# Optimization experiments

Measured on AMD Instinct MI355X. Metric: run time of the kernel, lower is better.

The kernel has to match this reference:

```python
import jax, jax.numpy as jnp
import numpy as np

N = 50000       # num_nodes
E = 800000      # num_edges (avg degree 16)
DIN = 128       # input_dim
DOUT = 128      # output_dim
H = 4           # num_heads
HD = DOUT // H  # head_dim = 32


def setup_inputs() -> dict:
    key = jax.random.key(0)
    ks = jax.random.split(key, 9)
    x = jax.random.normal(ks[0], (N, DIN), dtype=jnp.float32)
    edge_index = jax.random.randint(ks[1], (2, E), 0, N, dtype=jnp.int64)
    s = 1.0 / np.sqrt(DIN)
    Wq = jax.random.uniform(ks[2], (DOUT, DIN), jnp.float32, -s, s)
    bq = jax.random.uniform(ks[3], (DOUT,), jnp.float32, -s, s)
    Wk = jax.random.uniform(ks[4], (DOUT, DIN), jnp.float32, -s, s)
    bk = jax.random.uniform(ks[5], (DOUT,), jnp.float32, -s, s)
    Wv = jax.random.uniform(ks[6], (DOUT, DIN), jnp.float32, -s, s)
    bv = jax.random.uniform(ks[7], (DOUT,), jnp.float32, -s, s)
    att = jax.random.normal(ks[8], (H, 2 * HD), dtype=jnp.float32)  # nn.Parameter(randn)
    return {"x": x, "edge_index": edge_index, "Wq": Wq, "bq": bq,
            "Wk": Wk, "bk": bk, "Wv": Wv, "bv": bv, "att": att}


def reference(x, edge_index, Wq, bq, Wk, bk, Wv, bv, att):
    n = x.shape[0]
    q = (x @ Wq.T + bq).reshape(n, H, HD)
    k = (x @ Wk.T + bk).reshape(n, H, HD)
    v = (x @ Wv.T + bv).reshape(n, H, HD)
    row, col = edge_index[0], edge_index[1]

    # scores = leaky_relu(sum(cat([q[row],k[col]]) * att)) computed without concat
    a_q, a_k = att[:, :HD], att[:, HD:]                       # [H,HD] each
    scores = jnp.einsum('ehd,hd->eh', q[row], a_q) \
           + jnp.einsum('ehd,hd->eh', k[col], a_k)            # [E,H]
    scores = jax.nn.leaky_relu(scores, 0.2)

    # segment-softmax over edges grouped by destination node (col), per head
    m = jax.ops.segment_max(scores, col, num_segments=n)      # [N,H]
    m = jnp.where(jnp.isfinite(m), m, 0.0)                    # empty segments -> -inf guard
    e = jnp.exp(scores - m[col])                              # [E,H]
    denom = jax.ops.segment_sum(e, col, num_segments=n)       # [N,H]
    w_edge = e / denom[col]                                   # softmax per dst segment

    # attention_weights[i] = mean over incoming edges of softmax weights; 0 if deg==0
    deg = jax.ops.segment_sum(jnp.ones((col.shape[0],), jnp.float32), col,
                              num_segments=n)                 # [N]
    w_sum = jax.ops.segment_sum(w_edge, col, num_segments=n)  # [N,H]
    attn_w = jnp.where(deg[:, None] > 0, w_sum / jnp.maximum(deg, 1.0)[:, None], 0.0)

    # output[dst] += attn_w[dst] * v[src], summed over edges
    msgs = attn_w[col][:, :, None] * v[row]                   # [E,H,HD]
    out = jax.ops.segment_sum(msgs, col, num_segments=n)      # [N,H,HD]
    return out.reshape(n, DOUT)                               # dropout: eval mode (identity)
```

## Files before the change

### kernel.cpp

```cpp
#include <hip/hip_runtime.h>


#define N_NODES 50000
#define N_EDGES 800000
#define SPAN    96
#define NBUCK   521
#define CAP     2304
#define HSPAN   48
#define EPB     2048
#define NCHUNK  391
#define GEMMB   391

#define OFF_SORTED 12800000
#define OFF_CURSOR 17601536

typedef __attribute__((ext_vector_type(8))) short short8;
typedef __attribute__((ext_vector_type(4))) float f32x4;

__device__ __forceinline__ unsigned int pack_bf16_rne(float a, float b) {
    unsigned int ua = __float_as_uint(a), ub = __float_as_uint(b);
    unsigned int ha = (ua + 0x7FFFu + ((ua >> 16) & 1u)) >> 16;
    unsigned int hb = (ub + 0x7FFFu + ((ub >> 16) & 1u)) >> 16;
    return ha | (hb << 16);
}
__device__ __forceinline__ unsigned short bf16_rne(float a) {
    unsigned int ua = __float_as_uint(a);
    return (unsigned short)((ua + 0x7FFFu + ((ua >> 16) & 1u)) >> 16);
}
__device__ __forceinline__ float bflo(unsigned int u) { return __uint_as_float(u << 16); }
__device__ __forceinline__ float bfhi(unsigned int u) { return __uint_as_float(u & 0xFFFF0000u); }

__global__ __launch_bounds__(512) void fused_gemm_scatter(
        const float* __restrict__ x, const float* __restrict__ Wv,
        const float* __restrict__ bv, unsigned int* __restrict__ vh,
        const int* __restrict__ ei, unsigned int* __restrict__ Cursor,
        unsigned int* __restrict__ sorted) {
    __shared__ __align__(16) unsigned char smem[128 * 68 * 4];
    __shared__ int s_wide;
    int t = threadIdx.x;

    if (blockIdx.x < GEMMB) {
        unsigned int* wB = (unsigned int*)smem;
        for (int q = t; q < 8192; q += 512) {
            int o = q >> 6, k2 = q & 63;
            float2 wp = ((const float2*)Wv)[q];
            wB[o * 68 + k2] = pack_bf16_rne(wp.x, wp.y);
        }
        __syncthreads();

        int lane = t & 63, w = t >> 6;
        int quad = lane >> 4, lc = lane & 15;
        int n0 = blockIdx.x * 128 + w * 16;

        int arow = n0 + lc;
        int arowc = min(arow, N_NODES - 1);
        const float4* xrow = (const float4*)(x + (size_t)arowc * 128);

        f32x4 acc[8];
        #pragma unroll
        for (int ot = 0; ot < 8; ++ot) acc[ot] = (f32x4){0.f, 0.f, 0.f, 0.f};

        #pragma unroll
        for (int ks = 0; ks < 4; ++ks) {
            float4 f0 = xrow[ks * 8 + quad * 2];
            float4 f1 = xrow[ks * 8 + quad * 2 + 1];
            uint4 a4;
            a4.x = pack_bf16_rne(f0.x, f0.y);
            a4.y = pack_bf16_rne(f0.z, f0.w);
            a4.z = pack_bf16_rne(f1.x, f1.y);
            a4.w = pack_bf16_rne(f1.z, f1.w);
            short8 af = *(const short8*)&a4;
            #pragma unroll
            for (int ot = 0; ot < 8; ++ot) {
                uint4 b4 = *(const uint4*)&wB[(ot * 16 + lc) * 68 + ks * 16 + quad * 4];
                short8 bf = *(const short8*)&b4;
                acc[ot] = __builtin_amdgcn_mfma_f32_16x16x32_bf16(af, bf, acc[ot], 0, 0, 0);
            }
        }

        #pragma unroll
        for (int ot = 0; ot < 8; ++ot) {
            int o = ot * 16 + lc;
            float bb = bv[o];
            #pragma unroll
            for (int r = 0; r < 4; ++r) {
                int node = n0 + quad * 4 + r;
                unsigned short u = bf16_rne(acc[ot][r] + bb);
                unsigned int partner = (unsigned int)__shfl_xor((int)u, 1, 64);
                if ((lane & 1) == 0 && node < N_NODES) {
                    unsigned int pair = (unsigned int)u | (partner << 16);
                    vh[(size_t)node * 64 + (o >> 1)] = pair;
                }
            }
        }
    } else {
        unsigned int* w = (unsigned int*)smem;
        int* h    = (int*)(smem + EPB * 4);
        int* base = (int*)(smem + EPB * 4 + NBUCK * 4);
        unsigned int V = Cursor[NBUCK];
        for (int j = t; j < NBUCK; j += 512) h[j] = 0;
        if (t < 64) {
            int nz = (ei[2 * t + 1] != 0) ? 1 : 0;
            unsigned long long b = __ballot(nz);
            if (t == 0) s_wide = (b == 0ULL) ? 1 : 0;
        }
        __syncthreads();
        int wide = s_wide;
        int e0 = (blockIdx.x - GEMMB) * EPB;

        #pragma unroll
        for (int k = 0; k < EPB / 512; ++k) {
            int e = e0 + k * 512 + t;
            if (e < N_EDGES) {
                int r, c;
                if (wide) {
                    r = (int)((const uint2*)ei)[e].x;
                    c = (int)((const uint2*)ei)[N_EDGES + e].x;
                } else {
                    r = ei[e];
                    c = ei[N_EDGES + e];
                }
                w[k * 512 + t] = ((unsigned int)c << 16) | (unsigned int)r;
                atomicAdd(&h[c / SPAN], 1);
            } else {
                w[k * 512 + t] = 0xFFFFFFFFu;
            }
        }
        __syncthreads();
        for (int j = t; j < NBUCK; j += 512) {
            int cnt = h[j];
            base[j] = cnt ? (int)(atomicAdd(&Cursor[j], (unsigned int)cnt) - V) : 0;
            h[j] = 0;
        }
        __syncthreads();
        #pragma unroll
        for (int k = 0; k < EPB / 512; ++k) {
            unsigned int ww = w[k * 512 + t];
            if (ww != 0xFFFFFFFFu) {
                int bin = (int)(ww >> 16) / SPAN;
                int p = base[bin] + atomicAdd(&h[bin], 1);
                if (p >= 0 && p < CAP)
                    sorted[(size_t)bin * CAP + p] = ww;
            }
        }
    }
}

__global__ __launch_bounds__(512) void gather_kernel(const unsigned int* __restrict__ vh,
                                                     const unsigned int* __restrict__ sorted,
                                                     const unsigned int* __restrict__ Cursor,
                                                     float* __restrict__ out,
                                                     int ch) {
    __shared__ unsigned int ww[CAP];
    __shared__ unsigned short rl[CAP];
    __shared__ int deg[HSPAN];
    __shared__ int startc[HSPAN];
    __shared__ int curp[HSPAN];
    int t = threadIdx.x;
    int b  = blockIdx.x >> 1;
    int hb = blockIdx.x & 1;
    int nb0 = b * SPAN + hb * HSPAN;
    int span = min(HSPAN, N_NODES - nb0);
    if (span <= 0) return;
    unsigned int V = Cursor[NBUCK];
    int cnt = min((int)(Cursor[b] - V), CAP);
    if (t < HSPAN) deg[t] = 0;
    __syncthreads();

    const unsigned int* run = sorted + (size_t)b * CAP;
    for (int i = t; i < cnt; i += 512) {
        unsigned int v = run[i];
        ww[i] = v;
        unsigned int ln = (v >> 16) - (unsigned int)nb0;
        if (ln < (unsigned int)HSPAN) atomicAdd(&deg[ln], 1);
    }
    __syncthreads();

    if (t < 64) {
        int v = (t < HSPAN) ? deg[t] : 0;
        int s = v;
        #pragma unroll
        for (int off = 1; off < 64; off <<= 1) {
            int y = __shfl_up(s, off, 64);
            if (t >= off) s += y;
        }
        if (t < HSPAN) { startc[t] = s - v; curp[t] = 0; }
    }
    __syncthreads();

    for (int i = t; i < cnt; i += 512) {
        unsigned int v = ww[i];
        unsigned int ln = (v >> 16) - (unsigned int)nb0;
        if (ln < (unsigned int)HSPAN) {
            int p = startc[ln] + atomicAdd(&curp[ln], 1);
            rl[p] = (unsigned short)(v & 0xFFFFu);
        }
    }
    __syncthreads();

    int lane = t & 63, wid = t >> 6;
    int quad = lane >> 4;
    int li = lane & 15;
    const uint2* v2 = (const uint2*)(vh + (size_t)ch * 32);

#define ACC4(p) do { \
        c0 += (double)bflo((p).x); c1 += (double)bfhi((p).x); \
        c2 += (double)bflo((p).y); c3 += (double)bfhi((p).y); } while (0)

    for (int g = wid; g * 4 < span; g += 8) {
        int ln = g * 4 + quad;
        int s0 = startc[ln], d = deg[ln];
        double c0 = 0., c1 = 0., c2 = 0., c3 = 0.;
        int j = 0;
        if (d >= 8) {
            int a0 = rl[s0 + 0], a1 = rl[s0 + 1];
            int a2 = rl[s0 + 2], a3 = rl[s0 + 3];
            uint2 pA0 = v2[(size_t)a0 * 32 + li];
            uint2 pA1 = v2[(size_t)a1 * 32 + li];
            uint2 pA2 = v2[(size_t)a2 * 32 + li];
            uint2 pA3 = v2[(size_t)a3 * 32 + li];
            for (; j + 8 <= d; j += 4) {
                int b0 = rl[s0 + j + 4], b1 = rl[s0 + j + 5];
                int b2 = rl[s0 + j + 6], b3 = rl[s0 + j + 7];
                uint2 pB0 = v2[(size_t)b0 * 32 + li];
                uint2 pB1 = v2[(size_t)b1 * 32 + li];
                uint2 pB2 = v2[(size_t)b2 * 32 + li];
                uint2 pB3 = v2[(size_t)b3 * 32 + li];
                ACC4(pA0); ACC4(pA1); ACC4(pA2); ACC4(pA3);
                pA0 = pB0; pA1 = pB1; pA2 = pB2; pA3 = pB3;
            }
            ACC4(pA0); ACC4(pA1); ACC4(pA2); ACC4(pA3);
            j += 4;
        } else if (d >= 4) {
            int a0 = rl[s0 + 0], a1 = rl[s0 + 1];
            int a2 = rl[s0 + 2], a3 = rl[s0 + 3];
            uint2 pA0 = v2[(size_t)a0 * 32 + li];
            uint2 pA1 = v2[(size_t)a1 * 32 + li];
            uint2 pA2 = v2[(size_t)a2 * 32 + li];
            uint2 pA3 = v2[(size_t)a3 * 32 + li];
            ACC4(pA0); ACC4(pA1); ACC4(pA2); ACC4(pA3);
            j = 4;
        }
        for (; j < d; ++j) {
            int r0 = rl[s0 + j];
            uint2 p0 = v2[(size_t)r0 * 32 + li];
            ACC4(p0);
        }
        double sc = (d > 0) ? 1.0 / (double)d : 0.0;
        float4 ra = {(float)(c0 * sc), (float)(c1 * sc),
                     (float)(c2 * sc), (float)(c3 * sc)};
        ((float4*)out)[(size_t)(nb0 + ln) * 32 + ch * 16 + li] = ra;
    }
#undef ACC4
}

extern "C" void kernel_launch(void* const* d_in, const int* in_sizes, int n_in,
                              void* d_out, int out_size, void* d_ws, size_t ws_size,
                              hipStream_t stream) {
    const float* x  = (const float*)d_in[0];
    const int*   ei = (const int*)d_in[1];
    const float* Wv = (const float*)d_in[6];
    const float* bv = (const float*)d_in[7];
    float* out = (float*)d_out;

    char* ws = (char*)d_ws;
    unsigned int* vh     = (unsigned int*)(ws);
    unsigned int* sorted = (unsigned int*)(ws + OFF_SORTED);
    unsigned int* Cursor = (unsigned int*)(ws + OFF_CURSOR);

    fused_gemm_scatter<<<GEMMB + NCHUNK, 512, 0, stream>>>(x, Wv, bv, vh,
                                                           ei, Cursor, sorted);
    gather_kernel<<<NBUCK * 2, 512, 0, stream>>>(vh, sorted, Cursor, out, 0);
    gather_kernel<<<NBUCK * 2, 512, 0, stream>>>(vh, sorted, Cursor, out, 1);
}
```

Baseline: 150.2 us.

## Split gather into CSR build kernel plus column-sliced gather kernel

Replaces the two gather launches, which each rebuilt the per-node source list in shared memory, with one kernel that builds a global CSR (source ids plus packed degree/offset metadata) once. A new gather kernel then splits each node's 128 outputs into 8 slices of 16 columns, with 4 threads per node per slice, reading source ids from global memory. This removes the duplicated bucket sort work and raises parallelism. In exchange it adds a global round trip for the CSR, caps degree at 255 and each segment at HCAP entries, and has each thread gather less data per edge, so the gather is less coalesced.

```diff
diff --git a/kernel.cpp b/kernel.cpp
--- a/kernel.cpp
+++ b/kernel.cpp
@@ -7,12 +7,16 @@
 #define NBUCK   521
 #define CAP     2304
 #define HSPAN   48
+#define HCAP    1280
 #define EPB     2048
 #define NCHUNK  391
 #define GEMMB   391
+#define NB_G    391
 
 #define OFF_SORTED 12800000
 #define OFF_CURSOR 17601536
+#define OFF_RL     17604608
+#define OFF_META   20272128
 
 typedef __attribute__((ext_vector_type(8))) short short8;
 typedef __attribute__((ext_vector_type(4))) float f32x4;
@@ -146,13 +150,12 @@
     }
 }
 
-__global__ __launch_bounds__(512) void gather_kernel(const unsigned int* __restrict__ vh,
-                                                     const unsigned int* __restrict__ sorted,
-                                                     const unsigned int* __restrict__ Cursor,
-                                                     float* __restrict__ out,
-                                                     int ch) {
+__global__ __launch_bounds__(512) void csr_build(
+        const unsigned int* __restrict__ sorted,
+        const unsigned int* __restrict__ Cursor,
+        unsigned short* __restrict__ rl_g, unsigned int* __restrict__ meta) {
     __shared__ unsigned int ww[CAP];
-    __shared__ unsigned short rl[CAP];
+    __shared__ unsigned short rls[HCAP];
     __shared__ int deg[HSPAN];
     __shared__ int startc[HSPAN];
     __shared__ int curp[HSPAN];
@@ -160,8 +163,6 @@
     int b  = blockIdx.x >> 1;
     int hb = blockIdx.x & 1;
     int nb0 = b * SPAN + hb * HSPAN;
-    int span = min(HSPAN, N_NODES - nb0);
-    if (span <= 0) return;
     unsigned int V = Cursor[NBUCK];
     int cnt = min((int)(Cursor[b] - V), CAP);
     if (t < HSPAN) deg[t] = 0;
@@ -193,65 +194,84 @@
         unsigned int ln = (v >> 16) - (unsigned int)nb0;
         if (ln < (unsigned int)HSPAN) {
             int p = startc[ln] + atomicAdd(&curp[ln], 1);
-            rl[p] = (unsigned short)(v & 0xFFFFu);
-        }
-    }
-    __syncthreads();
-
-    int lane = t & 63, wid = t >> 6;
-    int quad = lane >> 4;
-    int li = lane & 15;
-    const uint2* v2 = (const uint2*)(vh + (size_t)ch * 32);
-
+            if (p < HCAP) rls[p] = (unsigned short)(v & 0xFFFFu);
+        }
+    }
+    __syncthreads();
+
+    unsigned int segbase = (unsigned int)(b * 2 + hb) * HCAP;
+    if (t < HSPAN) {
+        int node = nb0 + t;
+        if (node < N_NODES)
+            meta[node] = ((unsigned int)min(deg[t], 255) << 24)
+                       | (segbase + (unsigned int)startc[t]);
+    }
+    int total = min(startc[HSPAN - 1] + deg[HSPAN - 1], HCAP);
+    for (int i = t; i < total; i += 512)
+        rl_g[segbase + i] = rls[i];
+}
+
+__global__ __launch_bounds__(512) void gather_slice(
+        const unsigned int* __restrict__ vh,
+        const unsigned short* __restrict__ rl_g,
+        const unsigned int* __restrict__ meta, float* __restrict__ out) {
+    int t = threadIdx.x;
+    int slice = blockIdx.x & 7;
+    int node = (blockIdx.x >> 3) * 128 + (t >> 2);
+    int li = t & 2 ? (t & 3) : (t & 3);
+    li = t & 3;
+    unsigned int m = meta[min(node, N_NODES - 1)];
+    int d = (node < N_NODES) ? (int)(m >> 24) : 0;
+    unsigned int s0 = m & 0xFFFFFFu;
+    const uint2* v2 = (const uint2*)vh + slice * 4 + li;
+
+    double c0 = 0., c1 = 0., c2 = 0., c3 = 0.;
 #define ACC4(p) do { \
         c0 += (double)bflo((p).x); c1 += (double)bfhi((p).x); \
         c2 += (double)bflo((p).y); c3 += (double)bfhi((p).y); } while (0)
 
-    for (int g = wid; g * 4 < span; g += 8) {
-        int ln = g * 4 + quad;
-        int s0 = startc[ln], d = deg[ln];
-        double c0 = 0., c1 = 0., c2 = 0., c3 = 0.;
-        int j = 0;
-        if (d >= 8) {
-            int a0 = rl[s0 + 0], a1 = rl[s0 + 1];
-            int a2 = rl[s0 + 2], a3 = rl[s0 + 3];
-            uint2 pA0 = v2[(size_t)a0 * 32 + li];
-            uint2 pA1 = v2[(size_t)a1 * 32 + li];
-            uint2 pA2 = v2[(size_t)a2 * 32 + li];
-            uint2 pA3 = v2[(size_t)a3 * 32 + li];
-            for (; j + 8 <= d; j += 4) {
-                int b0 = rl[s0 + j + 4], b1 = rl[s0 + j + 5];
-                int b2 = rl[s0 + j + 6], b3 = rl[s0 + j + 7];
-                uint2 pB0 = v2[(size_t)b0 * 32 + li];
-                uint2 pB1 = v2[(size_t)b1 * 32 + li];
-                uint2 pB2 = v2[(size_t)b2 * 32 + li];
-                uint2 pB3 = v2[(size_t)b3 * 32 + li];
-                ACC4(pA0); ACC4(pA1); ACC4(pA2); ACC4(pA3);
-                pA0 = pB0; pA1 = pB1; pA2 = pB2; pA3 = pB3;
-            }
+    int j = 0;
+    if (d >= 8) {
+        int a0 = rl_g[s0 + 0], a1 = rl_g[s0 + 1];
+        int a2 = rl_g[s0 + 2], a3 = rl_g[s0 + 3];
+        uint2 pA0 = v2[(size_t)a0 * 32];
+        uint2 pA1 = v2[(size_t)a1 * 32];
+        uint2 pA2 = v2[(size_t)a2 * 32];
+        uint2 pA3 = v2[(size_t)a3 * 32];
+        for (; j + 8 <= d; j += 4) {
+            int b0 = rl_g[s0 + j + 4], b1 = rl_g[s0 + j + 5];
+            int b2 = rl_g[s0 + j + 6], b3 = rl_g[s0 + j + 7];
+            uint2 pB0 = v2[(size_t)b0 * 32];
+            uint2 pB1 = v2[(size_t)b1 * 32];
+            uint2 pB2 = v2[(size_t)b2 * 32];
+            uint2 pB3 = v2[(size_t)b3 * 32];
             ACC4(pA0); ACC4(pA1); ACC4(pA2); ACC4(pA3);
-            j += 4;
-        } else if (d >= 4) {
-            int a0 = rl[s0 + 0], a1 = rl[s0 + 1];
-            int a2 = rl[s0 + 2], a3 = rl[s0 + 3];
-            uint2 pA0 = v2[(size_t)a0 * 32 + li];
-            uint2 pA1 = v2[(size_t)a1 * 32 + li];
-            uint2 pA2 = v2[(size_t)a2 * 32 + li];
-            uint2 pA3 = v2[(size_t)a3 * 32 + li];
-            ACC4(pA0); ACC4(pA1); ACC4(pA2); ACC4(pA3);
-            j = 4;
-        }
-        for (; j < d; ++j) {
-            int r0 = rl[s0 + j];
-            uint2 p0 = v2[(size_t)r0 * 32 + li];
-            ACC4(p0);
-        }
+            pA0 = pB0; pA1 = pB1; pA2 = pB2; pA3 = pB3;
+        }
+        ACC4(pA0); ACC4(pA1); ACC4(pA2); ACC4(pA3);
+        j += 4;
+    } else if (d >= 4) {
+        int a0 = rl_g[s0 + 0], a1 = rl_g[s0 + 1];
+        int a2 = rl_g[s0 + 2], a3 = rl_g[s0 + 3];
+        uint2 pA0 = v2[(size_t)a0 * 32];
+        uint2 pA1 = v2[(size_t)a1 * 32];
+        uint2 pA2 = v2[(size_t)a2 * 32];
+        uint2 pA3 = v2[(size_t)a3 * 32];
+        ACC4(pA0); ACC4(pA1); ACC4(pA2); ACC4(pA3);
+        j = 4;
+    }
+    for (; j < d; ++j) {
+        int r0 = rl_g[s0 + j];
+        uint2 p0 = v2[(size_t)r0 * 32];
+        ACC4(p0);
+    }
+#undef ACC4
+    if (node < N_NODES) {
         double sc = (d > 0) ? 1.0 / (double)d : 0.0;
         float4 ra = {(float)(c0 * sc), (float)(c1 * sc),
                      (float)(c2 * sc), (float)(c3 * sc)};
-        ((float4*)out)[(size_t)(nb0 + ln) * 32 + ch * 16 + li] = ra;
-    }
-#undef ACC4
+        ((float4*)out)[(size_t)node * 32 + slice * 4 + li] = ra;
+    }
 }
 
 extern "C" void kernel_launch(void* const* d_in, const int* in_sizes, int n_in,
@@ -264,12 +284,14 @@
     float* out = (float*)d_out;
 
     char* ws = (char*)d_ws;
-    unsigned int* vh     = (unsigned int*)(ws);
-    unsigned int* sorted = (unsigned int*)(ws + OFF_SORTED);
-    unsigned int* Cursor = (unsigned int*)(ws + OFF_CURSOR);
+    unsigned int*   vh     = (unsigned int*)(ws);
+    unsigned int*   sorted = (unsigned int*)(ws + OFF_SORTED);
+    unsigned int*   Cursor = (unsigned int*)(ws + OFF_CURSOR);
+    unsigned short* rl_g   = (unsigned short*)(ws + OFF_RL);
+    unsigned int*   meta   = (unsigned int*)(ws + OFF_META);
 
     fused_gemm_scatter<<<GEMMB + NCHUNK, 512, 0, stream>>>(x, Wv, bv, vh,
                                                            ei, Cursor, sorted);
-    gather_kernel<<<NBUCK * 2, 512, 0, stream>>>(vh, sorted, Cursor, out, 0);
-    gather_kernel<<<NBUCK * 2, 512, 0, stream>>>(vh, sorted, Cursor, out, 1);
-}
+    csr_build<<<NBUCK * 2, 512, 0, stream>>>(sorted, Cursor, rl_g, meta);
+    gather_slice<<<NB_G * 8, 512, 0, stream>>>(vh, rl_g, meta, out);
+}
```

Measured after the change: 175.6 us. +17.0%, slower.
